# Kernel optimization log

Hardware: AMD Instinct MI355X
Metric: run time of the kernel (lower is better)

## Reference

```python
import jax, jax.numpy as jnp
import numpy as np

B, S, D = 1, 2048, 1024
F = 1408            # expert intermediate dim
E = 16              # num experts
K = 2               # top_k
CAP_FACTOR = 1.25


def _mlp(h, wg, wu, wd):
    # DeepSeek-style gated MLP (SwiGLU, no bias)
    return (jax.nn.silu(h @ wg) * (h @ wu)) @ wd


def setup_inputs() -> dict:
    key = jax.random.key(0)
    ks = jax.random.split(key, 10)
    sd = 0.02
    return {
        "x": jax.random.normal(ks[0], (B, S, D), jnp.float32),
        "router_w": jax.random.normal(ks[1], (D, E), jnp.float32) * sd,
        "router_b": jnp.zeros((E,), jnp.float32),
        "w_gate": jax.random.normal(ks[2], (E, D, F), jnp.float32) * sd,
        "w_up": jax.random.normal(ks[3], (E, D, F), jnp.float32) * sd,
        "w_down": jax.random.normal(ks[4], (E, F, D), jnp.float32) * sd,
        "sw_gate": jax.random.normal(ks[5], (D, F), jnp.float32) * sd,
        "sw_up": jax.random.normal(ks[6], (D, F), jnp.float32) * sd,
        "sw_down": jax.random.normal(ks[7], (F, D), jnp.float32) * sd,
    }


def reference(x, router_w, router_b, w_gate, w_up, w_down, sw_gate, sw_up, sw_down):
    b, s, d = x.shape
    N = b * s
    NK = N * K
    C = int(np.ceil(CAP_FACTOR * NK / E))  # per-expert capacity

    x_tokens = x.reshape(N, d)

    # Router: softmax -> top-k -> renormalize
    logits = x_tokens @ router_w + router_b           # [N, E]
    probs = jax.nn.softmax(logits, axis=-1)
    vals, idx = jax.lax.top_k(probs, K)               # [N, K]
    vals = vals / (jnp.sum(vals, axis=-1, keepdims=True) + 1e-9)
    idx_flat = idx.reshape(NK)                        # int expert ids
    vals_flat = vals.reshape(NK)

    # Position within each expert's buffer = rank in flattened (token, k) order.
    # Same math as (cumsum(one_hot)*one_hot).sum(-1)-1 in the original.
    oh_e = jax.nn.one_hot(idx_flat, E, dtype=x.dtype)             # [NK, E] (small)
    pos = (jnp.cumsum(oh_e, axis=0) * oh_e).sum(axis=1) - 1       # [NK]
    within = (pos < C).astype(x.dtype)                            # capacity mask
    pos_c = jnp.clip(pos, 0, C - 1).astype(jnp.int32)

    # Dispatch: scatter tokens into per-expert buffers. Positions are unique
    # per expert, so scatter-add equals the dense one-hot einsum exactly.
    token_ids = jnp.arange(NK) // K
    x_pair = x_tokens[token_ids] * within[:, None]                # [NK, D]
    expert_inputs = jnp.zeros((E, C, d), x.dtype).at[idx_flat, pos_c].add(x_pair)

    # Grouped expert MLPs
    expert_outputs = jax.vmap(_mlp)(expert_inputs, w_gate, w_up, w_down)  # [E, C, D]

    # Combine: gather back and weight by renormalized router probs
    gathered = expert_outputs[idx_flat, pos_c] * (vals_flat * within)[:, None]
    output_tokens = gathered.reshape(N, K, d).sum(axis=1)         # [N, D]

    return x + _mlp(x, sw_gate, sw_up, sw_down) + output_tokens.reshape(b, s, d)
```

## Files before the change

### kernel.cpp

```cpp
#include <hip/hip_runtime.h>
#include <hip/hip_bf16.h>

#define TOKENS 2048
#define DIM    1024
#define FDIM   1408
#define NEXP   16
#define NK     (TOKENS * 2)
#define CAP    320
#define RPAD   384

typedef __attribute__((ext_vector_type(4))) float f32x4;
typedef __attribute__((ext_vector_type(8))) short s16x8;
typedef __attribute__((ext_vector_type(4))) short s16x4;

__device__ __forceinline__ short f2bf(float f) {
    unsigned int u = __float_as_uint(f);
    u += 0x7FFFu + ((u >> 16) & 1u);
    return (short)(u >> 16);
}
__device__ __forceinline__ float bf2f(short s) {
    return __uint_as_float(((unsigned int)(unsigned short)s) << 16);
}
__device__ __forceinline__ unsigned int f2bf_pk(float lo, float hi) {
    union { __hip_bfloat162 h; unsigned int u; } c;
    c.h = __float22bfloat162_rn(make_float2(lo, hi));
    return c.u;
}

#define GLDS16(gp, lp) __builtin_amdgcn_global_load_lds(                     \
    (const __attribute__((address_space(1))) unsigned int*)(gp),             \
    (__attribute__((address_space(3))) unsigned int*)(lp), 16, 0, 0)

struct GSegW {
    const short* A; long aStride; int aRpad;
    const short* B0; const short* B1; long bStride;
    short* Out; long oStride; int oRpad;
    const int* cnt; int Mb, Nb, N, K, nblocks;
};
struct GSegB {
    const short* A; long aStride; int aRpad;
    const short* B0; long bStride;
    short* Out; long oStride;
    const int* cnt; int Mb, Nb, N, K, nblocks;
};
struct WSeg { const float* in; short* out; int K, N, mats, nblocks; };

__device__ void wchunk_dev(const WSeg& W, int bid)
{
    const int spm = W.K >> 3;
    const int mat = bid / spm, s = bid % spm;
    const float* in  = W.in  + (size_t)mat * W.K * W.N + (size_t)s * 8 * W.N;
    short* out = W.out + (size_t)mat * W.K * W.N + (size_t)s * W.N * 8;
    const int t = threadIdx.x;
    for (int n = t; n < W.N; n += 256) {
        float v[8];
#pragma unroll
        for (int j = 0; j < 8; j++) v[j] = in[(size_t)j * W.N + n];
        uint4 o;
        o.x = f2bf_pk(v[0], v[1]);
        o.y = f2bf_pk(v[2], v[3]);
        o.z = f2bf_pk(v[4], v[5]);
        o.w = f2bf_pk(v[6], v[7]);
        *(uint4*)(out + (size_t)n * 8) = o;
    }
}

__global__ __launch_bounds__(256) void router_kernel(
    const float* __restrict__ x, const float* __restrict__ rw,
    const float* __restrict__ rb, int* __restrict__ idx_flat,
    float* __restrict__ vals_flat)
{
    __shared__ float lg[16][17];
    const int t  = threadIdx.x;
    const int tl = t >> 4;
    const int e  = t & 15;
    const int token = blockIdx.x * 16 + tl;
    const float* xr = x + (size_t)token * DIM;

    float acc = 0.f;
    for (int d4 = 0; d4 < DIM / 4; d4++) {
        float4 xv = *(const float4*)(xr + d4 * 4);
        acc += xv.x * rw[(d4 * 4 + 0) * NEXP + e];
        acc += xv.y * rw[(d4 * 4 + 1) * NEXP + e];
        acc += xv.z * rw[(d4 * 4 + 2) * NEXP + e];
        acc += xv.w * rw[(d4 * 4 + 3) * NEXP + e];
    }
    lg[tl][e] = acc + rb[e];
    __syncthreads();

    if (t < 16) {
        float l[16];
#pragma unroll
        for (int j = 0; j < 16; j++) l[j] = lg[t][j];
        float m = l[0];
#pragma unroll
        for (int j = 1; j < 16; j++) m = fmaxf(m, l[j]);
        float p[16], den = 0.f;
#pragma unroll
        for (int j = 0; j < 16; j++) { p[j] = __expf(l[j] - m); den += p[j]; }
        int i1 = -1; float b1 = -1e30f;
#pragma unroll
        for (int j = 0; j < 16; j++) if (p[j] > b1) { b1 = p[j]; i1 = j; }
        int i2 = -1; float b2 = -1e30f;
#pragma unroll
        for (int j = 0; j < 16; j++) if (j != i1 && p[j] > b2) { b2 = p[j]; i2 = j; }
        float v1 = b1 / den, v2 = b2 / den;
        float s = v1 + v2 + 1e-9f;
        int tok = blockIdx.x * 16 + t;
        idx_flat[tok * 2 + 0] = i1;
        idx_flat[tok * 2 + 1] = i2;
        vals_flat[tok * 2 + 0] = v1 / s;
        vals_flat[tok * 2 + 1] = v2 / s;
    }
}

__global__ void scan_kernel(const int* __restrict__ idx_flat,
                            const float* __restrict__ vals,
                            int* __restrict__ dst, float* __restrict__ wgt,
                            int* __restrict__ cnt)
{
    const int lane = threadIdx.x;
    int base[16];
#pragma unroll
    for (int e = 0; e < 16; e++) base[e] = 0;

    for (int c = 0; c < NK / 64; c++) {
        int i = c * 64 + lane;
        int e = idx_flat[i];
        unsigned long long m[16];
#pragma unroll
        for (int ee = 0; ee < 16; ee++) m[ee] = __ballot(e == ee);
        unsigned long long mym = 0ULL; int myb = 0;
#pragma unroll
        for (int ee = 0; ee < 16; ee++) {
            bool sel = (e == ee);
            mym = sel ? m[ee] : mym;
            myb = sel ? base[ee] : myb;
        }
        int pos = myb + (int)__popcll(mym & ((1ULL << lane) - 1ULL));
        bool within = pos < CAP;
        dst[i] = within ? (e * RPAD + pos) : -1;
        wgt[i] = within ? vals[i] : 0.f;
#pragma unroll
        for (int ee = 0; ee < 16; ee++) base[ee] += (int)__popcll(m[ee]);
    }
    if (lane < 16) cnt[lane] = base[lane] < CAP ? base[lane] : CAP;
}

__device__ void xconv_dev(const float* __restrict__ x, short* __restrict__ xb, int bid)
{
    const int token = bid * 2 + (threadIdx.x >> 7);
    const int c = threadIdx.x & 127;
    const float* src = x + (size_t)token * DIM + c * 8;
    float4 v0 = *(const float4*)(src);
    float4 v1 = *(const float4*)(src + 4);
    s16x8 o;
    o[0] = f2bf(v0.x); o[1] = f2bf(v0.y); o[2] = f2bf(v0.z); o[3] = f2bf(v0.w);
    o[4] = f2bf(v1.x); o[5] = f2bf(v1.y); o[6] = f2bf(v1.z); o[7] = f2bf(v1.w);
    *(s16x8*)(xb + (size_t)c * (TOKENS * 8) + (size_t)token * 8) = o;
}

__device__ void scatter_dev(const float* __restrict__ x, const int* __restrict__ dst,
                            const int* __restrict__ idx_flat, short* __restrict__ ex,
                            int bid)
{
    const int i = bid * 2 + (threadIdx.x >> 7);
    const int d0 = dst[i];
    if (d0 < 0) return;
    const int e = idx_flat[i];
    const int pos = d0 - e * RPAD;
    const int token = i >> 1;
    const int c = threadIdx.x & 127;
    const float* src = x + (size_t)token * DIM + c * 8;
    float4 v0 = *(const float4*)(src);
    float4 v1 = *(const float4*)(src + 4);
    s16x8 o;
    o[0] = f2bf(v0.x); o[1] = f2bf(v0.y); o[2] = f2bf(v0.z); o[3] = f2bf(v0.w);
    o[4] = f2bf(v1.x); o[5] = f2bf(v1.y); o[6] = f2bf(v1.z); o[7] = f2bf(v1.w);
    *(s16x8*)(ex + (size_t)e * (DIM * RPAD) + (size_t)c * (RPAD * 8) +
              (size_t)pos * 8) = o;
}

__global__ __launch_bounds__(256) void prep_kernel(
    WSeg w0, WSeg w1, WSeg w2, WSeg w3,
    const float* __restrict__ x, short* __restrict__ xb,
    const int* __restrict__ dst, const int* __restrict__ idx_flat,
    short* __restrict__ ex)
{
    int bid = blockIdx.x;
    if (bid < w0.nblocks) { wchunk_dev(w0, bid); return; }
    bid -= w0.nblocks;
    if (bid < w1.nblocks) { wchunk_dev(w1, bid); return; }
    bid -= w1.nblocks;
    if (bid < w2.nblocks) { wchunk_dev(w2, bid); return; }
    bid -= w2.nblocks;
    if (bid < w3.nblocks) { wchunk_dev(w3, bid); return; }
    bid -= w3.nblocks;
    if (bid < TOKENS / 2) { xconv_dev(x, xb, bid); return; }
    bid -= TOKENS / 2;
    scatter_dev(x, dst, idx_flat, ex, bid);
}

template <int NMAT>
__device__ void gemm_glds128_dev(const GSegW& S, int bid)
{
    constexpr int BUFS = 4096 * (1 + NMAT);
    __shared__ short lds[3 * BUFS];

    const int cpx = S.nblocks >> 3;
    const int lid = (bid & 7) * cpx + (bid >> 3);
    const int mb  = lid % S.Mb;
    const int t1  = lid / S.Mb;
    const int nb  = t1 % S.Nb;
    const int g   = t1 / S.Nb;
    const int m0 = mb * 128, n0 = nb * 128;
    if (S.cnt != nullptr && m0 >= S.cnt[g]) return;

    const int tid = threadIdx.x, lane = tid & 63, w = tid >> 6;
    const int wr = w >> 1, wc = w & 1, ln = lane & 15, kg = lane >> 4;
    const int N = S.N, K = S.K;

    const short* Ag  = S.A  + (size_t)g * S.aStride + (size_t)m0 * 8;
    const short* Bg0 = S.B0 + (size_t)g * S.bStride + (size_t)n0 * 8;
    const short* Bg1 = nullptr;
    if constexpr (NMAT == 2) Bg1 = S.B1 + (size_t)g * S.bStride + (size_t)n0 * 8;

    const size_t aR8 = (size_t)S.aRpad * 8;
    const size_t n8  = (size_t)N * 8;

    const int srow = tid & 127, sslab = tid >> 7;
    const short* aS0 = Ag + sslab * aR8 + srow * 8;
    const short* aS1 = Ag + (2 + sslab) * aR8 + srow * 8;
    const short* bS00 = Bg0 + sslab * n8 + srow * 8;
    const short* bS01 = Bg0 + (2 + sslab) * n8 + srow * 8;
    const short *bS10 = nullptr, *bS11 = nullptr;
    if constexpr (NMAT == 2) {
        bS10 = Bg1 + sslab * n8 + srow * 8;
        bS11 = Bg1 + (2 + sslab) * n8 + srow * 8;
    }

    const int dA0 = w * 512, dA1 = 2048 + w * 512;

    auto STG = [&](int buf, int ks) {
        const size_t ka = (size_t)ks * 4 * aR8;
        const size_t kb = (size_t)ks * 4 * n8;
        short* base = lds + buf * BUFS;
        GLDS16(aS0 + ka,  base + dA0);
        GLDS16(aS1 + ka,  base + dA1);
        GLDS16(bS00 + kb, base + 4096 + dA0);
        GLDS16(bS01 + kb, base + 4096 + dA1);
        if constexpr (NMAT == 2) {
            GLDS16(bS10 + kb, base + 8192 + dA0);
            GLDS16(bS11 + kb, base + 8192 + dA1);
        }
    };

    const int aO = kg * 1024 + (wr * 64 + ln) * 8;
    const int bO = kg * 1024 + (wc * 64 + ln) * 8;

    f32x4 acc[NMAT][4][4] = {};
    const int nt = K / 32;
    STG(0, 0); STG(1, 1); STG(2, 2);
    int bb = 0;
    for (int ks = 0; ks < nt; ks++) {
        const int rem = nt - 1 - ks;
        if (rem >= 2) {
            if constexpr (NMAT == 2) asm volatile("s_waitcnt vmcnt(12)" ::: "memory");
            else                     asm volatile("s_waitcnt vmcnt(8)"  ::: "memory");
        } else if (rem == 1) {
            if constexpr (NMAT == 2) asm volatile("s_waitcnt vmcnt(6)" ::: "memory");
            else                     asm volatile("s_waitcnt vmcnt(4)" ::: "memory");
        } else {
            asm volatile("s_waitcnt vmcnt(0)" ::: "memory");
        }
        __builtin_amdgcn_s_barrier();
        __builtin_amdgcn_sched_barrier(0);

        const short* base = lds + bb * BUFS;
        s16x8 af[4];
#pragma unroll
        for (int m = 0; m < 4; m++)
            af[m] = *(const s16x8*)(base + aO + m * 128);
        s16x8 bf[NMAT][4];
#pragma unroll
        for (int mat = 0; mat < NMAT; mat++)
#pragma unroll
            for (int nf = 0; nf < 4; nf++)
                bf[mat][nf] = *(const s16x8*)(base + 4096 + mat * 4096 + bO + nf * 128);

        __builtin_amdgcn_s_setprio(1);
#pragma unroll
        for (int nf = 0; nf < 4; nf++)
#pragma unroll
            for (int m = 0; m < 4; m++)
#pragma unroll
                for (int mat = 0; mat < NMAT; mat++)
                    acc[mat][m][nf] = __builtin_amdgcn_mfma_f32_16x16x32_bf16(
                        af[m], bf[mat][nf], acc[mat][m][nf], 0, 0, 0);
        __builtin_amdgcn_s_setprio(0);
        __builtin_amdgcn_sched_barrier(0);
        __builtin_amdgcn_s_barrier();

        if (ks + 3 < nt) STG(bb, ks + 3);
        bb = (bb == 2) ? 0 : bb + 1;
    }

#pragma unroll
    for (int m = 0; m < 4; m++) {
#pragma unroll
        for (int nf = 0; nf < 4; nf++) {
            const int row = m0 + wr * 64 + m * 16 + kg * 4;
            const int col = n0 + wc * 64 + nf * 16 + ln;
#pragma unroll
            for (int j = 0; j < 4; j++) {
                if constexpr (NMAT == 2) {
                    float gv = acc[0][m][nf][j];
                    float uv = acc[1][m][nf][j];
                    float v = gv / (1.f + __expf(-gv)) * uv;
                    S.Out[(size_t)g * S.oStride + (size_t)(col >> 3) * (S.oRpad * 8) +
                          (size_t)(row + j) * 8 + (col & 7)] = f2bf(v);
                } else {
                    S.Out[(size_t)g * S.oStride + (size_t)(row + j) * N + col] =
                        f2bf(acc[0][m][nf][j]);
                }
            }
        }
    }
}

__device__ void gemm_glds64_dev(const GSegB& S, int bid)
{
    constexpr int BUFS = 6144;
    __shared__ short lds[2 * BUFS];

    const int cpx = S.nblocks >> 3;
    const int lid = (bid & 7) * cpx + (bid >> 3);
    const int mb  = lid % S.Mb;
    const int t1  = lid / S.Mb;
    const int nb  = t1 % S.Nb;
    const int g   = t1 / S.Nb;
    const int m0 = mb * 64, n0 = nb * 128;
    if (S.cnt != nullptr && m0 >= S.cnt[g]) return;

    const int tid = threadIdx.x, lane = tid & 63, w = tid >> 6;
    const int wr = w >> 1, wc = w & 1, ln = lane & 15, kg = lane >> 4;
    const int N = S.N, K = S.K;

    const short* Ag = S.A  + (size_t)g * S.aStride + (size_t)m0 * 8;
    const short* Bg = S.B0 + (size_t)g * S.bStride + (size_t)n0 * 8;

    const size_t aR8 = (size_t)S.aRpad * 8;
    const size_t n8  = (size_t)N * 8;

    const short* aS  = Ag + (size_t)(tid >> 6) * aR8 + (size_t)(tid & 63) * 8;
    const short* bS0 = Bg + (size_t)(tid >> 7) * n8 + (size_t)(tid & 127) * 8;
    const short* bS1 = Bg + (size_t)((tid >> 7) + 2) * n8 + (size_t)(tid & 127) * 8;

    const int dA  = w * 512;
    const int dB0 = 2048 + w * 512;
    const int dB1 = 4096 + w * 512;

    auto STG = [&](int buf, int ks) {
        const size_t ka = (size_t)ks * 4 * aR8;
        const size_t kb = (size_t)ks * 4 * n8;
        short* base = lds + buf * BUFS;
        GLDS16(aS + ka,  base + dA);
        GLDS16(bS0 + kb, base + dB0);
        GLDS16(bS1 + kb, base + dB1);
    };

    const int aO = kg * 512 + (wr * 32 + ln) * 8;
    const int bO = 2048 + kg * 1024 + (wc * 64 + ln) * 8;

    f32x4 acc[2][4] = {};
    const int nt = K / 32;
    STG(0, 0); STG(1, 1);
    int cur = 0;
    for (int ks = 0; ks < nt; ks++) {
        if (ks + 1 < nt) asm volatile("s_waitcnt vmcnt(3)" ::: "memory");
        else             asm volatile("s_waitcnt vmcnt(0)" ::: "memory");
        __builtin_amdgcn_s_barrier();
        __builtin_amdgcn_sched_barrier(0);

        const short* base = lds + cur * BUFS;
        s16x8 af[2];
        af[0] = *(const s16x8*)(base + aO);
        af[1] = *(const s16x8*)(base + aO + 128);
        s16x8 bf[4];
#pragma unroll
        for (int nf = 0; nf < 4; nf++)
            bf[nf] = *(const s16x8*)(base + bO + nf * 128);

#pragma unroll
        for (int nf = 0; nf < 4; nf++)
#pragma unroll
            for (int m = 0; m < 2; m++)
                acc[m][nf] = __builtin_amdgcn_mfma_f32_16x16x32_bf16(
                    af[m], bf[nf], acc[m][nf], 0, 0, 0);

        __builtin_amdgcn_sched_barrier(0);
        __builtin_amdgcn_s_barrier();
        if (ks + 2 < nt) STG(cur, ks + 2);
        cur ^= 1;
    }

#pragma unroll
    for (int m = 0; m < 2; m++) {
#pragma unroll
        for (int nf = 0; nf < 4; nf++) {
            const int row = m0 + wr * 32 + m * 16 + kg * 4;
            const int col = n0 + wc * 64 + nf * 16 + ln;
#pragma unroll
            for (int j = 0; j < 4; j++)
                S.Out[(size_t)g * S.oStride + (size_t)(row + j) * N + col] =
                    f2bf(acc[m][nf][j]);
        }
    }
}

__global__ __launch_bounds__(256, 2) void gateup_kernel(GSegW s0, GSegW s1,
                                                        WSeg w0, WSeg w1)
{
    int bid = blockIdx.x;
    if (bid < s0.nblocks) { gemm_glds128_dev<2>(s0, bid); return; }
    bid -= s0.nblocks;
    if (bid < s1.nblocks) { gemm_glds128_dev<2>(s1, bid); return; }
    bid -= s1.nblocks;
    if (bid < w0.nblocks) { wchunk_dev(w0, bid); return; }
    wchunk_dev(w1, bid - w0.nblocks);
}

__global__ __launch_bounds__(256, 4) void down_kernel(GSegB s0, GSegB s1)
{
    int bid = blockIdx.x;
    if (bid < s0.nblocks) { gemm_glds64_dev(s0, bid); return; }
    gemm_glds64_dev(s1, bid - s0.nblocks);
}

__global__ __launch_bounds__(256) void combine_kernel(
    const float* __restrict__ x, const short* __restrict__ shout,
    const short* __restrict__ eout, const int* __restrict__ dst,
    const float* __restrict__ wgt, float* __restrict__ out)
{
    const int t = blockIdx.x;
    const int d = threadIdx.x * 4;
    size_t o = (size_t)t * DIM + d;
    float4 xv = *(const float4*)(x + o);
    s16x4 sv = *(const s16x4*)(shout + o);
    float r0 = xv.x + bf2f(sv[0]);
    float r1 = xv.y + bf2f(sv[1]);
    float r2 = xv.z + bf2f(sv[2]);
    float r3 = xv.w + bf2f(sv[3]);
#pragma unroll
    for (int k = 0; k < 2; k++) {
        int di = dst[t * 2 + k];
        if (di >= 0) {
            float wv = wgt[t * 2 + k];
            s16x4 ev = *(const s16x4*)(eout + (size_t)di * DIM + d);
            r0 += wv * bf2f(ev[0]);
            r1 += wv * bf2f(ev[1]);
            r2 += wv * bf2f(ev[2]);
            r3 += wv * bf2f(ev[3]);
        }
    }
    float4 rv = {r0, r1, r2, r3};
    *(float4*)(out + o) = rv;
}

extern "C" void kernel_launch(void* const* d_in, const int* in_sizes, int n_in,
                              void* d_out, int out_size, void* d_ws, size_t ws_size,
                              hipStream_t stream)
{
    const float* x   = (const float*)d_in[0];
    const float* rw  = (const float*)d_in[1];
    const float* rb  = (const float*)d_in[2];
    const float* wg  = (const float*)d_in[3];
    const float* wu  = (const float*)d_in[4];
    const float* wd  = (const float*)d_in[5];
    const float* swg = (const float*)d_in[6];
    const float* swu = (const float*)d_in[7];
    const float* swd = (const float*)d_in[8];
    float* out = (float*)d_out;

    char* wp = (char*)d_ws;
    auto alloc = [&](size_t b) { char* p = wp; wp += (b + 255) & ~(size_t)255; return p; };
    int*   idx_flat = (int*)alloc((size_t)NK * 4);
    float* vals     = (float*)alloc((size_t)NK * 4);
    int*   dst      = (int*)alloc((size_t)NK * 4);
    float* wgt      = (float*)alloc((size_t)NK * 4);
    int*   cnt      = (int*)alloc(64);
    short* xb       = (short*)alloc((size_t)TOKENS * DIM * 2);
    short* ex       = (short*)alloc((size_t)NEXP * RPAD * DIM * 2);
    short* acte     = (short*)alloc((size_t)NEXP * RPAD * FDIM * 2);
    short* acts     = (short*)alloc((size_t)TOKENS * FDIM * 2);
    short* eout     = (short*)alloc((size_t)NEXP * RPAD * DIM * 2);
    short* shout    = (short*)alloc((size_t)TOKENS * DIM * 2);
    short* wgC      = (short*)alloc((size_t)NEXP * DIM * FDIM * 2);
    short* wuC      = (short*)alloc((size_t)NEXP * DIM * FDIM * 2);
    short* wdC      = (short*)alloc((size_t)NEXP * DIM * FDIM * 2);
    short* swgC     = (short*)alloc((size_t)DIM * FDIM * 2);
    short* swuC     = (short*)alloc((size_t)DIM * FDIM * 2);
    short* swdC     = (short*)alloc((size_t)DIM * FDIM * 2);

    router_kernel<<<TOKENS / 16, 256, 0, stream>>>(x, rw, rb, idx_flat, vals);
    scan_kernel<<<1, 64, 0, stream>>>(idx_flat, vals, dst, wgt, cnt);

    WSeg Wg  = {wg,  wgC,  DIM, FDIM, NEXP, NEXP * (DIM / 8)};
    WSeg Wu  = {wu,  wuC,  DIM, FDIM, NEXP, NEXP * (DIM / 8)};
    WSeg Wsg = {swg, swgC, DIM, FDIM, 1,    DIM / 8};
    WSeg Wsu = {swu, swuC, DIM, FDIM, 1,    DIM / 8};
    const int prep_blocks = Wg.nblocks + Wu.nblocks + Wsg.nblocks + Wsu.nblocks
                          + TOKENS / 2 + NK / 2;
    prep_kernel<<<prep_blocks, 256, 0, stream>>>(Wg, Wu, Wsg, Wsu,
                                                 x, xb, dst, idx_flat, ex);

    GSegW segGE = {ex, (long)RPAD * DIM, RPAD, wgC, wuC, (long)DIM * FDIM,
                   acte, (long)RPAD * FDIM, RPAD, cnt, 3, 11, FDIM, DIM, 3 * 11 * NEXP};
    GSegW segGS = {xb, 0L, TOKENS, swgC, swuC, 0L,
                   acts, 0L, TOKENS, nullptr, 16, 11, FDIM, DIM, 16 * 11};
    WSeg Wd  = {wd,  wdC,  FDIM, DIM, NEXP, NEXP * (FDIM / 8)};
    WSeg Wsd = {swd, swdC, FDIM, DIM, 1,    FDIM / 8};
    gateup_kernel<<<segGE.nblocks + segGS.nblocks + Wd.nblocks + Wsd.nblocks,
                    256, 0, stream>>>(segGE, segGS, Wd, Wsd);

    GSegB segDE = {acte, (long)RPAD * FDIM, RPAD, wdC, (long)DIM * FDIM,
                   eout, (long)RPAD * DIM, cnt, 6, 8, DIM, FDIM, 6 * 8 * NEXP};
    GSegB segDS = {acts, 0L, TOKENS, swdC, 0L,
                   shout, 0L, nullptr, 32, 8, DIM, FDIM, 32 * 8};
    down_kernel<<<segDE.nblocks + segDS.nblocks, 256, 0, stream>>>(segDE, segDS);

    combine_kernel<<<TOKENS, 256, 0, stream>>>(x, shout, eout, dst, wgt, out);
}
```

Measured before the change: 261.1 us.

## Pipeline weight conversion with gate/up GEMMs across four expert-group launches

Splits the expert gate/up phase into four launches of four experts each. Each launch also converts the fp32 gate/up weights of the next expert group and part of the down weights to bf16, so conversion overlaps with GEMM work instead of sitting in one large prep kernel ahead of it. The router and the x-to-bf16 conversion are merged into one launch, and the XCD block swizzle is generalised to block counts not divisible by 8. This adds more kernel launches and smaller per-launch grids, which may cost occupancy and tail time.

```diff
diff --git a/kernel.cpp b/kernel.cpp
--- a/kernel.cpp
+++ b/kernel.cpp
@@ -30,6 +30,12 @@
 #define GLDS16(gp, lp) __builtin_amdgcn_global_load_lds(                     \
     (const __attribute__((address_space(1))) unsigned int*)(gp),             \
     (__attribute__((address_space(3))) unsigned int*)(lp), 16, 0, 0)
+
+__device__ __forceinline__ int xcd_swz(int bid, int n) {
+    const int q = n >> 3, r = n & 7;
+    const int xcd = bid & 7, j = bid >> 3;
+    return (xcd < r) ? xcd * (q + 1) + j : r * (q + 1) + (xcd - r) * q + j;
+}
 
 struct GSegW {
     const short* A; long aStride; int aRpad;
@@ -43,7 +49,8 @@
     short* Out; long oStride;
     const int* cnt; int Mb, Nb, N, K, nblocks;
 };
-struct WSeg { const float* in; short* out; int K, N, mats, nblocks; };
+struct WSeg { const float* in; short* out; int K, N, nblocks; };
+struct ScSeg { const float* x; const int* dst; const int* idx; short* ex; int nblocks; };
 
 __device__ void wchunk_dev(const WSeg& W, int bid)
 {
@@ -65,16 +72,15 @@
     }
 }
 
-__global__ __launch_bounds__(256) void router_kernel(
-    const float* __restrict__ x, const float* __restrict__ rw,
-    const float* __restrict__ rb, int* __restrict__ idx_flat,
-    float* __restrict__ vals_flat)
+__device__ void router_dev(const float* __restrict__ x, const float* __restrict__ rw,
+                           const float* __restrict__ rb, int* __restrict__ idx_flat,
+                           float* __restrict__ vals_flat, int bid)
 {
     __shared__ float lg[16][17];
     const int t  = threadIdx.x;
     const int tl = t >> 4;
     const int e  = t & 15;
-    const int token = blockIdx.x * 16 + tl;
+    const int token = bid * 16 + tl;
     const float* xr = x + (size_t)token * DIM;
 
     float acc = 0.f;
@@ -106,45 +112,12 @@
         for (int j = 0; j < 16; j++) if (j != i1 && p[j] > b2) { b2 = p[j]; i2 = j; }
         float v1 = b1 / den, v2 = b2 / den;
         float s = v1 + v2 + 1e-9f;
-        int tok = blockIdx.x * 16 + t;
+        int tok = bid * 16 + t;
         idx_flat[tok * 2 + 0] = i1;
         idx_flat[tok * 2 + 1] = i2;
         vals_flat[tok * 2 + 0] = v1 / s;
         vals_flat[tok * 2 + 1] = v2 / s;
     }
-}
-
-__global__ void scan_kernel(const int* __restrict__ idx_flat,
-                            const float* __restrict__ vals,
-                            int* __restrict__ dst, float* __restrict__ wgt,
-                            int* __restrict__ cnt)
-{
-    const int lane = threadIdx.x;
-    int base[16];
-#pragma unroll
-    for (int e = 0; e < 16; e++) base[e] = 0;
-
-    for (int c = 0; c < NK / 64; c++) {
-        int i = c * 64 + lane;
-        int e = idx_flat[i];
-        unsigned long long m[16];
-#pragma unroll
-        for (int ee = 0; ee < 16; ee++) m[ee] = __ballot(e == ee);
-        unsigned long long mym = 0ULL; int myb = 0;
-#pragma unroll
-        for (int ee = 0; ee < 16; ee++) {
-            bool sel = (e == ee);
-            mym = sel ? m[ee] : mym;
-            myb = sel ? base[ee] : myb;
-        }
-        int pos = myb + (int)__popcll(mym & ((1ULL << lane) - 1ULL));
-        bool within = pos < CAP;
-        dst[i] = within ? (e * RPAD + pos) : -1;
-        wgt[i] = within ? vals[i] : 0.f;
-#pragma unroll
-        for (int ee = 0; ee < 16; ee++) base[ee] += (int)__popcll(m[ee]);
-    }
-    if (lane < 16) cnt[lane] = base[lane] < CAP ? base[lane] : CAP;
 }
 
 __device__ void xconv_dev(const float* __restrict__ x, short* __restrict__ xb, int bid)
@@ -160,32 +133,70 @@
     *(s16x8*)(xb + (size_t)c * (TOKENS * 8) + (size_t)token * 8) = o;
 }
 
-__device__ void scatter_dev(const float* __restrict__ x, const int* __restrict__ dst,
-                            const int* __restrict__ idx_flat, short* __restrict__ ex,
-                            int bid)
+__global__ __launch_bounds__(256) void rx_kernel(
+    const float* __restrict__ x, const float* __restrict__ rw,
+    const float* __restrict__ rb, int* __restrict__ idx_flat,
+    float* __restrict__ vals, short* __restrict__ xb)
+{
+    int bid = blockIdx.x;
+    if (bid < TOKENS / 16) { router_dev(x, rw, rb, idx_flat, vals, bid); return; }
+    xconv_dev(x, xb, bid - TOKENS / 16);
+}
+
+__global__ void scan_kernel(const int* __restrict__ idx_flat,
+                            const float* __restrict__ vals,
+                            int* __restrict__ dst, float* __restrict__ wgt,
+                            int* __restrict__ cnt)
+{
+    const int lane = threadIdx.x;
+    int base[16];
+#pragma unroll
+    for (int e = 0; e < 16; e++) base[e] = 0;
+
+    for (int c = 0; c < NK / 64; c++) {
+        int i = c * 64 + lane;
+        int e = idx_flat[i];
+        unsigned long long m[16];
+#pragma unroll
+        for (int ee = 0; ee < 16; ee++) m[ee] = __ballot(e == ee);
+        unsigned long long mym = 0ULL; int myb = 0;
+#pragma unroll
+        for (int ee = 0; ee < 16; ee++) {
+            bool sel = (e == ee);
+            mym = sel ? m[ee] : mym;
+            myb = sel ? base[ee] : myb;
+        }
+        int pos = myb + (int)__popcll(mym & ((1ULL << lane) - 1ULL));
+        bool within = pos < CAP;
+        dst[i] = within ? (e * RPAD + pos) : -1;
+        wgt[i] = within ? vals[i] : 0.f;
+#pragma unroll
+        for (int ee = 0; ee < 16; ee++) base[ee] += (int)__popcll(m[ee]);
+    }
+    if (lane < 16) cnt[lane] = base[lane] < CAP ? base[lane] : CAP;
+}
+
+__device__ void scatter_dev(const ScSeg& S, int bid)
 {
     const int i = bid * 2 + (threadIdx.x >> 7);
-    const int d0 = dst[i];
+    const int d0 = S.dst[i];
     if (d0 < 0) return;
-    const int e = idx_flat[i];
+    const int e = S.idx[i];
     const int pos = d0 - e * RPAD;
     const int token = i >> 1;
     const int c = threadIdx.x & 127;
-    const float* src = x + (size_t)token * DIM + c * 8;
+    const float* src = S.x + (size_t)token * DIM + c * 8;
     float4 v0 = *(const float4*)(src);
     float4 v1 = *(const float4*)(src + 4);
     s16x8 o;
     o[0] = f2bf(v0.x); o[1] = f2bf(v0.y); o[2] = f2bf(v0.z); o[3] = f2bf(v0.w);
     o[4] = f2bf(v1.x); o[5] = f2bf(v1.y); o[6] = f2bf(v1.z); o[7] = f2bf(v1.w);
-    *(s16x8*)(ex + (size_t)e * (DIM * RPAD) + (size_t)c * (RPAD * 8) +
+    *(s16x8*)(S.ex + (size_t)e * (DIM * RPAD) + (size_t)c * (RPAD * 8) +
               (size_t)pos * 8) = o;
 }
 
 __global__ __launch_bounds__(256) void prep_kernel(
-    WSeg w0, WSeg w1, WSeg w2, WSeg w3,
-    const float* __restrict__ x, short* __restrict__ xb,
-    const int* __restrict__ dst, const int* __restrict__ idx_flat,
-    short* __restrict__ ex)
+    WSeg w0, WSeg w1, WSeg w2, WSeg w3, WSeg w4, ScSeg sc)
 {
     int bid = blockIdx.x;
     if (bid < w0.nblocks) { wchunk_dev(w0, bid); return; }
@@ -196,9 +207,9 @@
     bid -= w2.nblocks;
     if (bid < w3.nblocks) { wchunk_dev(w3, bid); return; }
     bid -= w3.nblocks;
-    if (bid < TOKENS / 2) { xconv_dev(x, xb, bid); return; }
-    bid -= TOKENS / 2;
-    scatter_dev(x, dst, idx_flat, ex, bid);
+    if (bid < w4.nblocks) { wchunk_dev(w4, bid); return; }
+    bid -= w4.nblocks;
+    if (bid < sc.nblocks) scatter_dev(sc, bid);
 }
 
 template <int NMAT>
@@ -207,8 +218,7 @@
     constexpr int BUFS = 4096 * (1 + NMAT);
     __shared__ short lds[3 * BUFS];
 
-    const int cpx = S.nblocks >> 3;
-    const int lid = (bid & 7) * cpx + (bid >> 3);
+    const int lid = xcd_swz(bid, S.nblocks);
     const int mb  = lid % S.Mb;
     const int t1  = lid / S.Mb;
     const int nb  = t1 % S.Nb;
@@ -333,8 +343,7 @@
     constexpr int BUFS = 6144;
     __shared__ short lds[2 * BUFS];
 
-    const int cpx = S.nblocks >> 3;
-    const int lid = (bid & 7) * cpx + (bid >> 3);
+    const int lid = xcd_swz(bid, S.nblocks);
     const int mb  = lid % S.Mb;
     const int t1  = lid / S.Mb;
     const int nb  = t1 % S.Nb;
@@ -418,16 +427,19 @@
     }
 }
 
-__global__ __launch_bounds__(256, 2) void gateup_kernel(GSegW s0, GSegW s1,
-                                                        WSeg w0, WSeg w1)
+__global__ __launch_bounds__(256, 2) void megaGU_kernel(
+    GSegW g0, GSegW g1, WSeg w0, WSeg w1, WSeg w2)
 {
     int bid = blockIdx.x;
-    if (bid < s0.nblocks) { gemm_glds128_dev<2>(s0, bid); return; }
-    bid -= s0.nblocks;
-    if (bid < s1.nblocks) { gemm_glds128_dev<2>(s1, bid); return; }
-    bid -= s1.nblocks;
+    if (bid < g0.nblocks) { gemm_glds128_dev<2>(g0, bid); return; }
+    bid -= g0.nblocks;
+    if (bid < g1.nblocks) { gemm_glds128_dev<2>(g1, bid); return; }
+    bid -= g1.nblocks;
     if (bid < w0.nblocks) { wchunk_dev(w0, bid); return; }
-    wchunk_dev(w1, bid - w0.nblocks);
+    bid -= w0.nblocks;
+    if (bid < w1.nblocks) { wchunk_dev(w1, bid); return; }
+    bid -= w1.nblocks;
+    if (bid < w2.nblocks) wchunk_dev(w2, bid);
 }
 
 __global__ __launch_bounds__(256, 4) void down_kernel(GSegB s0, GSegB s1)
@@ -502,26 +514,62 @@
     short* swuC     = (short*)alloc((size_t)DIM * FDIM * 2);
     short* swdC     = (short*)alloc((size_t)DIM * FDIM * 2);
 
-    router_kernel<<<TOKENS / 16, 256, 0, stream>>>(x, rw, rb, idx_flat, vals);
+    const size_t WGU = (size_t)DIM * FDIM;
+    const int spmGU = DIM / 8;
+    const int spmWD = FDIM / 8;
+
+    auto wseg = [&](const float* in, short* outp, int e0, int ne, int K, int N,
+                    int spm) {
+        WSeg s = {in + (size_t)e0 * K * N, outp + (size_t)e0 * K * N, K, N,
+                  ne * spm};
+        return s;
+    };
+    auto guE = [&](int e0) {
+        GSegW s = {ex + (size_t)e0 * RPAD * DIM, (long)RPAD * DIM, RPAD,
+                   wgC + (size_t)e0 * WGU, wuC + (size_t)e0 * WGU, (long)WGU,
+                   acte + (size_t)e0 * RPAD * FDIM, (long)RPAD * FDIM, RPAD,
+                   cnt + e0, 3, 11, FDIM, DIM, 3 * 11 * 4};
+        return s;
+    };
+    auto guS = [&](int qi) {
+        GSegW s = {xb + (size_t)qi * 512 * 8, 0L, TOKENS,
+                   swgC, swuC, 0L,
+                   acts + (size_t)qi * 512 * 8, 0L, TOKENS,
+                   nullptr, 4, 11, FDIM, DIM, 4 * 11};
+        return s;
+    };
+    WSeg wnull = {nullptr, nullptr, 8, 0, 0};
+
+    rx_kernel<<<TOKENS / 16 + TOKENS / 2, 256, 0, stream>>>(x, rw, rb,
+                                                            idx_flat, vals, xb);
     scan_kernel<<<1, 64, 0, stream>>>(idx_flat, vals, dst, wgt, cnt);
 
-    WSeg Wg  = {wg,  wgC,  DIM, FDIM, NEXP, NEXP * (DIM / 8)};
-    WSeg Wu  = {wu,  wuC,  DIM, FDIM, NEXP, NEXP * (DIM / 8)};
-    WSeg Wsg = {swg, swgC, DIM, FDIM, 1,    DIM / 8};
-    WSeg Wsu = {swu, swuC, DIM, FDIM, 1,    DIM / 8};
-    const int prep_blocks = Wg.nblocks + Wu.nblocks + Wsg.nblocks + Wsu.nblocks
-                          + TOKENS / 2 + NK / 2;
-    prep_kernel<<<prep_blocks, 256, 0, stream>>>(Wg, Wu, Wsg, Wsu,
-                                                 x, xb, dst, idx_flat, ex);
-
-    GSegW segGE = {ex, (long)RPAD * DIM, RPAD, wgC, wuC, (long)DIM * FDIM,
-                   acte, (long)RPAD * FDIM, RPAD, cnt, 3, 11, FDIM, DIM, 3 * 11 * NEXP};
-    GSegW segGS = {xb, 0L, TOKENS, swgC, swuC, 0L,
-                   acts, 0L, TOKENS, nullptr, 16, 11, FDIM, DIM, 16 * 11};
-    WSeg Wd  = {wd,  wdC,  FDIM, DIM, NEXP, NEXP * (FDIM / 8)};
-    WSeg Wsd = {swd, swdC, FDIM, DIM, 1,    FDIM / 8};
-    gateup_kernel<<<segGE.nblocks + segGS.nblocks + Wd.nblocks + Wsd.nblocks,
-                    256, 0, stream>>>(segGE, segGS, Wd, Wsd);
+    {
+        WSeg a = {swg, swgC, DIM, FDIM, spmGU};
+        WSeg b = {swu, swuC, DIM, FDIM, spmGU};
+        WSeg c = wseg(wg, wgC, 0, 4, DIM, FDIM, spmGU);
+        WSeg d = wseg(wu, wuC, 0, 4, DIM, FDIM, spmGU);
+        WSeg e = {swd, swdC, FDIM, DIM, spmWD};
+        ScSeg sc = {x, dst, idx_flat, ex, NK / 2};
+        const int nb = a.nblocks + b.nblocks + c.nblocks + d.nblocks +
+                       e.nblocks + sc.nblocks;
+        prep_kernel<<<nb, 256, 0, stream>>>(a, b, c, d, e, sc);
+    }
+
+    for (int i = 0; i < 4; i++) {
+        GSegW g0 = guE(4 * i);
+        GSegW g1 = guS(i);
+        WSeg a = wnull, b = wnull, c = wnull;
+        if (i < 3) {
+            a = wseg(wg, wgC, 4 * (i + 1), 4, DIM, FDIM, spmGU);
+            b = wseg(wu, wuC, 4 * (i + 1), 4, DIM, FDIM, spmGU);
+        }
+        if (i == 0)      c = wseg(wd, wdC, 0, 5, FDIM, DIM, spmWD);
+        else if (i == 1) c = wseg(wd, wdC, 5, 5, FDIM, DIM, spmWD);
+        else if (i == 2) c = wseg(wd, wdC, 10, 6, FDIM, DIM, spmWD);
+        const int nb = g0.nblocks + g1.nblocks + a.nblocks + b.nblocks + c.nblocks;
+        megaGU_kernel<<<nb, 256, 0, stream>>>(g0, g1, a, b, c);
+    }
 
     GSegB segDE = {acte, (long)RPAD * FDIM, RPAD, wdC, (long)DIM * FDIM,
                    eout, (long)RPAD * DIM, cnt, 6, 8, DIM, FDIM, 6 * 8 * NEXP};
```

Result: slower. 278.6 us (+6.7%).
